# Kernel optimization log

Hardware: AMD Instinct MI355X
Metric: run time of the kernel (lower is better)

Reference implementation:

```python
import jax, jax.numpy as jnp
import numpy as np

N_NODES = 131072
N_EDGES = 2097152
F_IN = 128
G_NODES = 256  # nodes per graph (equal-size graphs -> ptr = arange(0, N+1, 256))


def _linear(x, W, b):
    return x @ W + b


def _gin_conv(x, src, dst, W1, b1, W2, b2):
    # GINConv with eps=0: MLP(x + sum_{j->i} x_j)
    agg = jax.ops.segment_sum(x[src], dst, num_segments=x.shape[0])
    h = jax.nn.relu(_linear(x + agg, W1, b1))
    return _linear(h, W2, b2)


def _init(key, fan_in, fan_out):
    kw, kb = jax.random.split(key)
    s = 1.0 / np.sqrt(fan_in)
    W = jax.random.uniform(kw, (fan_in, fan_out), jnp.float32, -s, s)
    b = jax.random.uniform(kb, (fan_out,), jnp.float32, -s, s)
    return W, b


def setup_inputs() -> dict:
    key = jax.random.key(0)
    ks = jax.random.split(key, 14)
    x = jax.random.normal(ks[0], (N_NODES, F_IN), jnp.float32)
    edge_index = jax.random.randint(ks[1], (2, N_EDGES), 0, N_NODES, jnp.int64)
    W1a, b1a = _init(ks[2], F_IN, 128)
    W2a, b2a = _init(ks[3], 128, 128)
    W1b, b1b = _init(ks[4], 128, 128)
    W2b, b2b = _init(ks[5], 128, 128)
    Ws1, bs1 = _init(ks[6], 128, 32)
    Ws2, bs2 = _init(ks[7], 32, 32)
    Ws3, bs3 = _init(ks[8], 32, 32)
    Wm1, bm1 = _init(ks[9], 32 * 32, 32)
    Wm2, bm2 = _init(ks[10], 32, 32)
    Wm3, bm3 = _init(ks[11], 32, 2)
    return dict(x=x, edge_index=edge_index,
                W1a=W1a, b1a=b1a, W2a=W2a, b2a=b2a,
                W1b=W1b, b1b=b1b, W2b=W2b, b2b=b2b,
                Ws1=Ws1, bs1=bs1, Ws2=Ws2, bs2=bs2, Ws3=Ws3, bs3=bs3,
                Wm1=Wm1, bm1=bm1, Wm2=Wm2, bm2=bm2, Wm3=Wm3, bm3=bm3,
                nodes_per_graph=G_NODES)


def reference(x, edge_index, W1a, b1a, W2a, b2a, W1b, b1b, W2b, b2b,
              Ws1, bs1, Ws2, bs2, Ws3, bs3,
              Wm1, bm1, Wm2, bm2, Wm3, bm3, nodes_per_graph):
    src, dst = edge_index[0], edge_index[1]
    # two GINConv layers, each followed by outer ReLU (as in forward)
    h = jax.nn.relu(_gin_conv(x, src, dst, W1a, b1a, W2a, b2a))
    h = jax.nn.relu(_gin_conv(h, src, dst, W1b, b1b, W2b, b2b))
    # dropout is identity in eval mode; F.normalize(dim=1) row-wise L2
    hn = h / jnp.maximum(jnp.linalg.norm(h, axis=1, keepdims=True), 1e-12)
    s = jax.nn.relu(_linear(hn, Ws1, bs1))
    s = jax.nn.relu(_linear(s, Ws2, bs2))
    s = jax.nn.relu(_linear(s, Ws3, bs3))  # [N, 32]
    G = x.shape[0] // nodes_per_graph
    sg = s.reshape(G, nodes_per_graph, 32)
    # per-graph second-order pooling: graph.T @ graph, flattened
    HH = jnp.einsum('gnf,gne->gfe', sg, sg).reshape(G, 32 * 32)  # [G, 1024]
    o = jax.nn.relu(_linear(HH, Wm1, bm1))
    o = jax.nn.relu(_linear(o, Wm2, bm2))
    out = jax.nn.relu(_linear(o, Wm3, bm3))  # [G, 2]; output dropout identity in eval
    return (HH, out)
```

## Files before the change

### kernel.cpp

```cpp
#include <hip/hip_runtime.h>
#include <hip/hip_bf16.h>


#define NN 131072
#define NE 2097152
#define NG 512
#define NB 1024
#define BCAP 4096
#define ECH 8192
#define CAP 3072

typedef unsigned short u16;
typedef unsigned int u32;
typedef __attribute__((ext_vector_type(8))) short short8;
typedef __attribute__((ext_vector_type(4))) float f32x4;

__device__ __forceinline__ float bf2f(u16 u) {
    union { u32 i; float f; } x; x.i = ((u32)u) << 16; return x.f;
}
__device__ __forceinline__ u16 f2bf(float f) {
    union { u32 i; float f; } x; x.f = f;
    u32 r = x.i + 0x7fffu + ((x.i >> 16) & 1u);
    return (u16)(r >> 16);
}

__global__ __launch_bounds__(256) void cast_x(const float* __restrict__ xf,
                                              u16* __restrict__ xb) {
    int i = blockIdx.x * 256 + threadIdx.x;
    const float4* src = (const float4*)xf;
    float4 a = src[2 * i], b = src[2 * i + 1];
    uint4 o;
    o.x = (u32)f2bf(a.x) | ((u32)f2bf(a.y) << 16);
    o.y = (u32)f2bf(a.z) | ((u32)f2bf(a.w) << 16);
    o.z = (u32)f2bf(b.x) | ((u32)f2bf(b.y) << 16);
    o.w = (u32)f2bf(b.z) | ((u32)f2bf(b.w) << 16);
    ((uint4*)xb)[i] = o;
}

__global__ __launch_bounds__(256) void init_cursor(int* __restrict__ cursor) {
    int b = blockIdx.x * 256 + threadIdx.x;
    cursor[b] = b * BCAP;
}

__global__ __launch_bounds__(256) void bin_scatter(const int* __restrict__ gsrc,
                                                   const int* __restrict__ gdst,
                                                   int* __restrict__ cursor,
                                                   u32* __restrict__ ebuf) {
    __shared__ int lc[NB];
    __shared__ int rb[NB];
    __shared__ int lb[NB];
    int t = threadIdx.x;
    for (int i = 0; i < 4; ++i) lc[t + i * 256] = 0;
    __syncthreads();
    int base = blockIdx.x * ECH;
    for (int i = 0; i < ECH / 256; ++i) {
        int d = gdst[base + i * 256 + t];
        atomicAdd(&lc[d >> 7], 1);
    }
    __syncthreads();
    for (int i = 0; i < 4; ++i) {
        int b = t + i * 256;
        int c = lc[b];
        rb[b] = c ? atomicAdd(&cursor[b], c) : 0;
        lb[b] = 0;
    }
    __syncthreads();
    for (int i = 0; i < ECH / 256; ++i) {
        int idx = base + i * 256 + t;
        int d = gdst[idx];
        int s = gsrc[idx];
        int b = d >> 7;
        int o = atomicAdd(&lb[b], 1);
        ebuf[rb[b] + o] = ((u32)s << 7) | (u32)(d & 127);
    }
}

__global__ __launch_bounds__(512) void aggregate_bucket(const u16* __restrict__ X,
                                                        const u32* __restrict__ ebuf,
                                                        const int* __restrict__ bcur,
                                                        u16* __restrict__ T) {
    __shared__ int lcnt[128];
    __shared__ int lstart[128];
    __shared__ int lofs[128];
    __shared__ int sorted[CAP];
    int t = threadIdx.x, lane = t & 63, wave = t >> 6;
    int bkt = blockIdx.x;
    const u32* Xu = (const u32*)X;

    float a0[16], a1[16];
#pragma unroll
    for (int i = 0; i < 16; ++i) {
        int row = bkt * 128 + wave * 16 + i;
        u32 v = Xu[(size_t)row * 64 + lane];
        a0[i] = bf2f((u16)v);
        a1[i] = bf2f((u16)(v >> 16));
    }

    int e0 = bkt * BCAP, e1 = bcur[bkt];
    for (int cs = e0; cs < e1; cs += CAP) {
        int n = min(CAP, e1 - cs);
        if (t < 128) lcnt[t] = 0;
        __syncthreads();
        for (int j = t; j < n; j += 512)
            atomicAdd(&lcnt[ebuf[cs + j] & 127], 1);
        __syncthreads();
        if (wave == 0) {
            int c0 = lcnt[2 * lane], c1 = lcnt[2 * lane + 1];
            int s = c0 + c1, e = s;
            for (int o = 1; o < 64; o <<= 1) {
                int u = __shfl_up(e, o, 64);
                if (lane >= o) e += u;
            }
            int excl = e - s;
            lstart[2 * lane] = excl;          lofs[2 * lane] = excl;
            lstart[2 * lane + 1] = excl + c0; lofs[2 * lane + 1] = excl + c0;
        }
        __syncthreads();
        for (int j = t; j < n; j += 512) {
            u32 e = ebuf[cs + j];
            int pos = atomicAdd(&lofs[e & 127], 1);
            sorted[pos] = (int)(e >> 7);
        }
        __syncthreads();
#pragma unroll
        for (int i = 0; i < 16; ++i) {
            int node = wave * 16 + i;
            int p = lstart[node], pe = p + lcnt[node];
            for (; p < pe; p += 8) {
                int s[8]; float m[8];
#pragma unroll
                for (int k = 0; k < 8; ++k) {
                    int q = p + k;
                    s[k] = sorted[q < pe ? q : pe - 1];
                    m[k] = (q < pe) ? 1.f : 0.f;
                }
                u32 w[8];
#pragma unroll
                for (int k = 0; k < 8; ++k) w[k] = Xu[(size_t)s[k] * 64 + lane];
#pragma unroll
                for (int k = 0; k < 8; ++k) {
                    a0[i] = fmaf(m[k], bf2f((u16)w[k]), a0[i]);
                    a1[i] = fmaf(m[k], bf2f((u16)(w[k] >> 16)), a1[i]);
                }
            }
        }
        __syncthreads();
    }

    u32* Tu = (u32*)T;
#pragma unroll
    for (int i = 0; i < 16; ++i) {
        int row = bkt * 128 + wave * 16 + i;
        Tu[(size_t)row * 64 + lane] = (u32)f2bf(a0[i]) | ((u32)f2bf(a1[i]) << 16);
    }
}

__global__ __launch_bounds__(256) void transpose_w(const float* a, const float* b,
                                                   const float* c, const float* d, u16* Wt) {
    const float* w = (blockIdx.x == 0) ? a : (blockIdx.x == 1) ? b : (blockIdx.x == 2) ? c : d;
    u16* o = Wt + blockIdx.x * 16384;
    for (int i = 0; i < 64; ++i) {
        int idx = threadIdx.x + i * 256;
        o[(idx & 127) * 128 + (idx >> 7)] = f2bf(w[idx]);
    }
}

__global__ __launch_bounds__(256) void transpose_small(const float* Ws1, const float* Ws2,
                                                       const float* Ws3, u16* Wsm) {
    int t = threadIdx.x;
    for (int i = 0; i < 16; ++i) {
        int idx = t + i * 256;
        int k = idx >> 5, n = idx & 31;
        Wsm[n * 128 + k] = f2bf(Ws1[idx]);
    }
    for (int i = 0; i < 4; ++i) {
        int idx = t + i * 256;
        int k = idx >> 5, n = idx & 31;
        Wsm[4096 + n * 32 + k] = f2bf(Ws2[idx]);
        Wsm[5120 + n * 32 + k] = f2bf(Ws3[idx]);
    }
}

__global__ __launch_bounds__(256) void gemm2_relu(const u16* __restrict__ A,
                                                  const u16* __restrict__ Wt1,
                                                  const u16* __restrict__ Wt2,
                                                  const float* __restrict__ b1,
                                                  const float* __restrict__ b2,
                                                  u16* __restrict__ C) {
    __shared__ u16 As[64][136];
    __shared__ u16 Ws[128][136];
    int tid = threadIdx.x;
    size_t rowBase = (size_t)blockIdx.x * 64;

    uint4 w2r[8];
#pragma unroll
    for (int i = 0; i < 8; ++i) {
        int c = tid + i * 256;
        w2r[i] = *(const uint4*)(Wt2 + (c >> 4) * 128 + ((c & 15) << 3));
    }
    for (int i = 0; i < 4; ++i) {
        int c = tid + i * 256;
        int r = c >> 4, co = (c & 15) << 3;
        *(uint4*)&As[r][co] = *(const uint4*)(A + (rowBase + r) * 128 + co);
    }
    for (int i = 0; i < 8; ++i) {
        int c = tid + i * 256;
        int r = c >> 4, co = (c & 15) << 3;
        *(uint4*)&Ws[r][co] = *(const uint4*)(Wt1 + r * 128 + co);
    }
    __syncthreads();

    int lane = tid & 63, wave = tid >> 6;
    int quad = lane >> 4, l16 = lane & 15;

    f32x4 acc[8];
#pragma unroll
    for (int t = 0; t < 8; ++t) acc[t] = (f32x4){0.f, 0.f, 0.f, 0.f};
#pragma unroll
    for (int c = 0; c < 4; ++c) {
        short8 a = *(const short8*)&As[wave * 16 + l16][c * 32 + quad * 8];
#pragma unroll
        for (int t = 0; t < 8; ++t) {
            short8 b = *(const short8*)&Ws[t * 16 + l16][c * 32 + quad * 8];
            acc[t] = __builtin_amdgcn_mfma_f32_16x16x32_bf16(a, b, acc[t], 0, 0, 0);
        }
    }

#pragma unroll
    for (int t = 0; t < 8; ++t) {
        int col = t * 16 + l16;
        float bv = b1[col];
#pragma unroll
        for (int r = 0; r < 4; ++r)
            As[wave * 16 + quad * 4 + r][col] = f2bf(fmaxf(acc[t][r] + bv, 0.f));
    }
    __syncthreads();

#pragma unroll
    for (int i = 0; i < 8; ++i) {
        int c = tid + i * 256;
        *(uint4*)&Ws[c >> 4][(c & 15) << 3] = w2r[i];
    }
    __syncthreads();

    f32x4 acc2[8];
#pragma unroll
    for (int t = 0; t < 8; ++t) acc2[t] = (f32x4){0.f, 0.f, 0.f, 0.f};
#pragma unroll
    for (int c = 0; c < 4; ++c) {
        short8 a = *(const short8*)&As[wave * 16 + l16][c * 32 + quad * 8];
#pragma unroll
        for (int t = 0; t < 8; ++t) {
            short8 b = *(const short8*)&Ws[t * 16 + l16][c * 32 + quad * 8];
            acc2[t] = __builtin_amdgcn_mfma_f32_16x16x32_bf16(a, b, acc2[t], 0, 0, 0);
        }
    }
#pragma unroll
    for (int t = 0; t < 8; ++t) {
        int col = t * 16 + l16;
        float bv = b2[col];
#pragma unroll
        for (int r = 0; r < 4; ++r) {
            int row = wave * 16 + quad * 4 + r;
            C[(rowBase + row) * 128 + col] = f2bf(fmaxf(acc2[t][r] + bv, 0.f));
        }
    }
}

__global__ __launch_bounds__(256) void norm_mlp_mfma(const u16* __restrict__ X,
                                                     const u16* __restrict__ Wsm,
                                                     const float* __restrict__ bs1,
                                                     const float* __restrict__ bs2,
                                                     const float* __restrict__ bs3,
                                                     float* __restrict__ S) {
    __shared__ u16 As[64][136];
    __shared__ u16 W1s[32][136];
    __shared__ u16 W23s[2][32][40];
    __shared__ u16 H[64][40];
    int tid = threadIdx.x, lane = tid & 63, wave = tid >> 6;
    int quad = lane >> 4, l16 = lane & 15;
    size_t rowBase = (size_t)blockIdx.x * 64;

#pragma unroll
    for (int i = 0; i < 2; ++i) {
        int c = tid + i * 256;
        int r = c >> 4, co = (c & 15) << 3;
        *(uint4*)&W1s[r][co] = *(const uint4*)(Wsm + r * 128 + co);
    }
    {
        int which = tid >> 7, cc = tid & 127;
        int r = cc >> 2, co = (cc & 3) << 3;
        *(uint4*)&W23s[which][r][co] = *(const uint4*)(Wsm + 4096 + which * 1024 + r * 32 + co);
    }

    const u32* Xu = (const u32*)X;
    for (int i = 0; i < 16; ++i) {
        int row = wave * 16 + i;
        u32 v = Xu[(rowBase + row) * 64 + lane];
        float f0 = bf2f((u16)v), f1 = bf2f((u16)(v >> 16));
        float ss = f0 * f0 + f1 * f1;
        for (int o = 1; o < 64; o <<= 1) ss += __shfl_xor(ss, o, 64);
        float inv = 1.0f / fmaxf(sqrtf(ss), 1e-12f);
        *(u32*)&As[row][2 * lane] = (u32)f2bf(f0 * inv) | ((u32)f2bf(f1 * inv) << 16);
    }
    __syncthreads();

    f32x4 acc[2];
    acc[0] = (f32x4){0.f, 0.f, 0.f, 0.f};
    acc[1] = (f32x4){0.f, 0.f, 0.f, 0.f};
#pragma unroll
    for (int c = 0; c < 4; ++c) {
        short8 a = *(const short8*)&As[wave * 16 + l16][c * 32 + quad * 8];
#pragma unroll
        for (int t = 0; t < 2; ++t) {
            short8 b = *(const short8*)&W1s[t * 16 + l16][c * 32 + quad * 8];
            acc[t] = __builtin_amdgcn_mfma_f32_16x16x32_bf16(a, b, acc[t], 0, 0, 0);
        }
    }
#pragma unroll
    for (int t = 0; t < 2; ++t) {
        int col = t * 16 + l16;
        float bv = bs1[col];
#pragma unroll
        for (int r = 0; r < 4; ++r)
            H[wave * 16 + quad * 4 + r][col] = f2bf(fmaxf(acc[t][r] + bv, 0.f));
    }
    __syncthreads();

    f32x4 acc2[2];
    acc2[0] = (f32x4){0.f, 0.f, 0.f, 0.f};
    acc2[1] = (f32x4){0.f, 0.f, 0.f, 0.f};
    {
        short8 a = *(const short8*)&H[wave * 16 + l16][quad * 8];
#pragma unroll
        for (int t = 0; t < 2; ++t) {
            short8 b = *(const short8*)&W23s[0][t * 16 + l16][quad * 8];
            acc2[t] = __builtin_amdgcn_mfma_f32_16x16x32_bf16(a, b, acc2[t], 0, 0, 0);
        }
    }
    __syncthreads();
#pragma unroll
    for (int t = 0; t < 2; ++t) {
        int col = t * 16 + l16;
        float bv = bs2[col];
#pragma unroll
        for (int r = 0; r < 4; ++r)
            H[wave * 16 + quad * 4 + r][col] = f2bf(fmaxf(acc2[t][r] + bv, 0.f));
    }
    __syncthreads();

    f32x4 acc3[2];
    acc3[0] = (f32x4){0.f, 0.f, 0.f, 0.f};
    acc3[1] = (f32x4){0.f, 0.f, 0.f, 0.f};
    {
        short8 a = *(const short8*)&H[wave * 16 + l16][quad * 8];
#pragma unroll
        for (int t = 0; t < 2; ++t) {
            short8 b = *(const short8*)&W23s[1][t * 16 + l16][quad * 8];
            acc3[t] = __builtin_amdgcn_mfma_f32_16x16x32_bf16(a, b, acc3[t], 0, 0, 0);
        }
    }
#pragma unroll
    for (int t = 0; t < 2; ++t) {
        int col = t * 16 + l16;
        float bv = bs3[col];
#pragma unroll
        for (int r = 0; r < 4; ++r) {
            int row = wave * 16 + quad * 4 + r;
            S[(rowBase + row) * 32 + col] = fmaxf(acc3[t][r] + bv, 0.f);
        }
    }
}

__global__ __launch_bounds__(256) void gram(const float* __restrict__ S,
                                            float* __restrict__ out) {
    __shared__ float Sg[256 * 32];
    int t = threadIdx.x, g = blockIdx.x;
    const float4* src = (const float4*)(S + (size_t)g * 8192);
    float4* dst = (float4*)Sg;
    for (int i = 0; i < 8; ++i) dst[t + i * 256] = src[t + i * 256];
    __syncthreads();

    int f = t >> 3, e0 = (t & 7) << 2;
    float4 a = {0.f, 0.f, 0.f, 0.f};
    for (int n = 0; n < 256; ++n) {
        float sf = Sg[n * 32 + f];
        float4 se = *(const float4*)&Sg[n * 32 + e0];
        a.x += sf * se.x; a.y += sf * se.y; a.z += sf * se.z; a.w += sf * se.w;
    }
    *(float4*)(out + (size_t)g * 1024 + f * 32 + e0) = a;
}

__global__ __launch_bounds__(256) void graph_mlp(const float* __restrict__ HH,
                                                 const float* Wm1, const float* bm1,
                                                 const float* Wm2, const float* bm2,
                                                 const float* Wm3, const float* bm3,
                                                 float* __restrict__ out) {
    __shared__ float hh[1024];
    __shared__ float red[256];
    __shared__ float o1[32];
    __shared__ float o2[32];
    int t = threadIdx.x, g = blockIdx.x;
    ((float4*)hh)[t] = ((const float4*)(HH + (size_t)g * 1024))[t];
    __syncthreads();

    int j = t & 31, part = t >> 5;
    float p = 0.f;
    for (int i = 0; i < 128; ++i) { int k = part * 128 + i; p += hh[k] * Wm1[k * 32 + j]; }
    red[t] = p;
    __syncthreads();
    if (t < 32) {
        float s = 0.f;
        for (int q = 0; q < 8; ++q) s += red[q * 32 + t];
        o1[t] = fmaxf(s + bm1[t], 0.f);
    }
    __syncthreads();
    if (t < 32) {
        float s = 0.f;
        for (int k = 0; k < 32; ++k) s += o1[k] * Wm2[k * 32 + t];
        o2[t] = fmaxf(s + bm2[t], 0.f);
    }
    __syncthreads();
    if (t < 2) {
        float s = 0.f;
        for (int k = 0; k < 32; ++k) s += o2[k] * Wm3[k * 2 + t];
        out[524288 + g * 2 + t] = fmaxf(s + bm3[t], 0.f);
    }
}

extern "C" void kernel_launch(void* const* d_in, const int* in_sizes, int n_in,
                              void* d_out, int out_size, void* d_ws, size_t ws_size,
                              hipStream_t stream) {
    const float* x   = (const float*)d_in[0];
    const int*   ei  = (const int*)d_in[1];
    const float* W1a = (const float*)d_in[2];  const float* b1a = (const float*)d_in[3];
    const float* W2a = (const float*)d_in[4];  const float* b2a = (const float*)d_in[5];
    const float* W1b = (const float*)d_in[6];  const float* b1b = (const float*)d_in[7];
    const float* W2b = (const float*)d_in[8];  const float* b2b = (const float*)d_in[9];
    const float* Ws1 = (const float*)d_in[10]; const float* bs1 = (const float*)d_in[11];
    const float* Ws2 = (const float*)d_in[12]; const float* bs2 = (const float*)d_in[13];
    const float* Ws3 = (const float*)d_in[14]; const float* bs3 = (const float*)d_in[15];
    const float* Wm1 = (const float*)d_in[16]; const float* bm1 = (const float*)d_in[17];
    const float* Wm2 = (const float*)d_in[18]; const float* bm2 = (const float*)d_in[19];
    const float* Wm3 = (const float*)d_in[20]; const float* bm3 = (const float*)d_in[21];
    float* out = (float*)d_out;

    const int* gsrc = ei;
    const int* gdst = ei + NE;

    char* ws = (char*)d_ws;
    size_t off = 0;
    auto alloc = [&](size_t bytes) { size_t r = off; off = (off + bytes + 255) & ~(size_t)255; return r; };
    int*  cursor = (int*)(ws + alloc((size_t)NB * 4));
    u32*  ebuf   = (u32*)(ws + alloc((size_t)NB * BCAP * 4));
    u16*  Wt     = (u16*)(ws + alloc(4 * 16384 * 2));
    u16*  Wsm    = (u16*)(ws + alloc(6144 * 2));
    u16*  X0     = (u16*)(ws + alloc((size_t)NN * 128 * 2));
    u16*  B1     = (u16*)(ws + alloc((size_t)NN * 128 * 2));
    float* S     = (float*)B1;
    (void)ws_size; (void)n_in; (void)in_sizes; (void)out_size;

    init_cursor<<<NB / 256, 256, 0, stream>>>(cursor);
    bin_scatter<<<NE / ECH, 256, 0, stream>>>(gsrc, gdst, cursor, ebuf);

    cast_x<<<NN * 128 / (256 * 8), 256, 0, stream>>>(x, X0);
    transpose_w<<<4, 256, 0, stream>>>(W1a, W2a, W1b, W2b, Wt);
    transpose_small<<<1, 256, 0, stream>>>(Ws1, Ws2, Ws3, Wsm);

    aggregate_bucket<<<NB, 512, 0, stream>>>(X0, ebuf, cursor, B1);
    gemm2_relu<<<NN / 64, 256, 0, stream>>>(B1, Wt + 0 * 16384, Wt + 1 * 16384, b1a, b2a, X0);
    aggregate_bucket<<<NB, 512, 0, stream>>>(X0, ebuf, cursor, B1);
    gemm2_relu<<<NN / 64, 256, 0, stream>>>(B1, Wt + 2 * 16384, Wt + 3 * 16384, b1b, b2b, X0);

    norm_mlp_mfma<<<NN / 64, 256, 0, stream>>>(X0, Wsm, bs1, bs2, bs3, S);
    gram<<<NG, 256, 0, stream>>>(S, out);
    graph_mlp<<<NG, 256, 0, stream>>>(out, Wm1, bm1, Wm2, bm2, Wm3, bm3, out);
}
```

Measured before the change: 499.4 us.

## Build padded CSR once and fuse aggregation into GIN MLP kernel

Adds a csr_sort kernel that sorts each bucket's edges by destination once into a padded CSR. Padding entries point to a zeroed sentinel row NN, so the gather loop needs no masking. The per-layer bucket sort is dropped, and the neighbour-sum gather is fused into the two-GEMM MLP kernel, which now works on 128-row tiles with 512 threads. This removes the per-layer re-sort, the bf16 intermediate write and reload, and a kernel launch. In exchange it adds capacity limits (ECAP/CCAP) that could overflow on skewed degree distributions, and the fused kernel may lose occupancy.

```diff
diff --git a/kernel.cpp b/kernel.cpp
--- a/kernel.cpp
+++ b/kernel.cpp
@@ -6,9 +6,9 @@
 #define NE 2097152
 #define NG 512
 #define NB 1024
-#define BCAP 4096
+#define ECAP 2560
+#define CCAP 3328
 #define ECH 8192
-#define CAP 3072
 
 typedef unsigned short u16;
 typedef unsigned int u32;
@@ -37,9 +37,17 @@
     ((uint4*)xb)[i] = o;
 }
 
+__global__ __launch_bounds__(128) void zero_tail(u16* __restrict__ X0,
+                                                 u16* __restrict__ H1) {
+    int t = threadIdx.x;
+    u32* a = (u32*)(X0 + (size_t)NN * 128);
+    u32* b = (u32*)(H1 + (size_t)NN * 128);
+    if (t < 64) a[t] = 0; else b[t - 64] = 0;
+}
+
 __global__ __launch_bounds__(256) void init_cursor(int* __restrict__ cursor) {
     int b = blockIdx.x * 256 + threadIdx.x;
-    cursor[b] = b * BCAP;
+    cursor[b] = b * ECAP;
 }
 
 __global__ __launch_bounds__(256) void bin_scatter(const int* __restrict__ gsrc,
@@ -75,83 +83,50 @@
     }
 }
 
-__global__ __launch_bounds__(512) void aggregate_bucket(const u16* __restrict__ X,
-                                                        const u32* __restrict__ ebuf,
-                                                        const int* __restrict__ bcur,
-                                                        u16* __restrict__ T) {
+__global__ __launch_bounds__(512) void csr_sort(const u32* __restrict__ ebuf,
+                                                const int* __restrict__ cursor,
+                                                int* __restrict__ csr,
+                                                int* __restrict__ start,
+                                                int* __restrict__ deg) {
     __shared__ int lcnt[128];
     __shared__ int lstart[128];
     __shared__ int lofs[128];
-    __shared__ int sorted[CAP];
     int t = threadIdx.x, lane = t & 63, wave = t >> 6;
     int bkt = blockIdx.x;
-    const u32* Xu = (const u32*)X;
-
-    float a0[16], a1[16];
-#pragma unroll
-    for (int i = 0; i < 16; ++i) {
-        int row = bkt * 128 + wave * 16 + i;
-        u32 v = Xu[(size_t)row * 64 + lane];
-        a0[i] = bf2f((u16)v);
-        a1[i] = bf2f((u16)(v >> 16));
-    }
-
-    int e0 = bkt * BCAP, e1 = bcur[bkt];
-    for (int cs = e0; cs < e1; cs += CAP) {
-        int n = min(CAP, e1 - cs);
-        if (t < 128) lcnt[t] = 0;
-        __syncthreads();
-        for (int j = t; j < n; j += 512)
-            atomicAdd(&lcnt[ebuf[cs + j] & 127], 1);
-        __syncthreads();
-        if (wave == 0) {
-            int c0 = lcnt[2 * lane], c1 = lcnt[2 * lane + 1];
-            int s = c0 + c1, e = s;
-            for (int o = 1; o < 64; o <<= 1) {
-                int u = __shfl_up(e, o, 64);
-                if (lane >= o) e += u;
-            }
-            int excl = e - s;
-            lstart[2 * lane] = excl;          lofs[2 * lane] = excl;
-            lstart[2 * lane + 1] = excl + c0; lofs[2 * lane + 1] = excl + c0;
-        }
-        __syncthreads();
-        for (int j = t; j < n; j += 512) {
-            u32 e = ebuf[cs + j];
-            int pos = atomicAdd(&lofs[e & 127], 1);
-            sorted[pos] = (int)(e >> 7);
-        }
-        __syncthreads();
-#pragma unroll
-        for (int i = 0; i < 16; ++i) {
-            int node = wave * 16 + i;
-            int p = lstart[node], pe = p + lcnt[node];
-            for (; p < pe; p += 8) {
-                int s[8]; float m[8];
-#pragma unroll
-                for (int k = 0; k < 8; ++k) {
-                    int q = p + k;
-                    s[k] = sorted[q < pe ? q : pe - 1];
-                    m[k] = (q < pe) ? 1.f : 0.f;
-                }
-                u32 w[8];
-#pragma unroll
-                for (int k = 0; k < 8; ++k) w[k] = Xu[(size_t)s[k] * 64 + lane];
-#pragma unroll
-                for (int k = 0; k < 8; ++k) {
-                    a0[i] = fmaf(m[k], bf2f((u16)w[k]), a0[i]);
-                    a1[i] = fmaf(m[k], bf2f((u16)(w[k] >> 16)), a1[i]);
-                }
-            }
-        }
-        __syncthreads();
-    }
-
-    u32* Tu = (u32*)T;
-#pragma unroll
-    for (int i = 0; i < 16; ++i) {
-        int row = bkt * 128 + wave * 16 + i;
-        Tu[(size_t)row * 64 + lane] = (u32)f2bf(a0[i]) | ((u32)f2bf(a1[i]) << 16);
+    int e0 = bkt * ECAP;
+    int n = cursor[bkt] - e0;
+    if (t < 128) lcnt[t] = 0;
+    __syncthreads();
+    for (int j = t; j < n; j += 512)
+        atomicAdd(&lcnt[ebuf[e0 + j] & 127], 1);
+    __syncthreads();
+    if (wave == 0) {
+        int c0 = lcnt[2 * lane], c1 = lcnt[2 * lane + 1];
+        int r0 = (c0 + 7) & ~7, r1 = (c1 + 7) & ~7;
+        int s = r0 + r1, e = s;
+        for (int o = 1; o < 64; o <<= 1) {
+            int u = __shfl_up(e, o, 64);
+            if (lane >= o) e += u;
+        }
+        int excl = e - s;
+        lstart[2 * lane] = excl;          lofs[2 * lane] = excl;
+        lstart[2 * lane + 1] = excl + r0; lofs[2 * lane + 1] = excl + r0;
+    }
+    __syncthreads();
+    for (int j = t; j < n; j += 512) {
+        u32 e = ebuf[e0 + j];
+        int node = e & 127;
+        int pos = atomicAdd(&lofs[node], 1);
+        csr[bkt * CCAP + pos] = (int)(e >> 7);
+    }
+    __syncthreads();
+    if (t < 128) {
+        int c = lcnt[t];
+        int cp = (c + 7) & ~7;
+        int base = bkt * CCAP + lstart[t];
+        for (int q = c; q < cp; ++q) csr[base + q] = NN;
+        start[bkt * 128 + t] = base;
+        deg[bkt * 128 + t] = cp;
     }
 }
 
@@ -181,37 +156,58 @@
     }
 }
 
-__global__ __launch_bounds__(256) void gemm2_relu(const u16* __restrict__ A,
+__global__ __launch_bounds__(512, 4) void agg_mlp(const u16* __restrict__ X,
+                                                  const int* __restrict__ csr,
+                                                  const int* __restrict__ start,
+                                                  const int* __restrict__ deg,
                                                   const u16* __restrict__ Wt1,
                                                   const u16* __restrict__ Wt2,
                                                   const float* __restrict__ b1,
                                                   const float* __restrict__ b2,
                                                   u16* __restrict__ C) {
-    __shared__ u16 As[64][136];
+    __shared__ u16 As[128][136];
     __shared__ u16 Ws[128][136];
-    int tid = threadIdx.x;
-    size_t rowBase = (size_t)blockIdx.x * 64;
-
-    uint4 w2r[8];
-#pragma unroll
-    for (int i = 0; i < 8; ++i) {
-        int c = tid + i * 256;
-        w2r[i] = *(const uint4*)(Wt2 + (c >> 4) * 128 + ((c & 15) << 3));
-    }
+    int tid = threadIdx.x, lane = tid & 63, wave = tid >> 6;
+    int quad = lane >> 4, l16 = lane & 15;
+    size_t rowBase = (size_t)blockIdx.x * 128;
+    const u32* Xu = (const u32*)X;
+
+#pragma unroll
     for (int i = 0; i < 4; ++i) {
-        int c = tid + i * 256;
-        int r = c >> 4, co = (c & 15) << 3;
-        *(uint4*)&As[r][co] = *(const uint4*)(A + (rowBase + r) * 128 + co);
-    }
-    for (int i = 0; i < 8; ++i) {
-        int c = tid + i * 256;
+        int c = tid + i * 512;
         int r = c >> 4, co = (c & 15) << 3;
         *(uint4*)&Ws[r][co] = *(const uint4*)(Wt1 + r * 128 + co);
     }
-    __syncthreads();
-
-    int lane = tid & 63, wave = tid >> 6;
-    int quad = lane >> 4, l16 = lane & 15;
+
+    for (int i = 0; i < 16; ++i) {
+        int row = (int)rowBase + wave * 16 + i;
+        u32 v = Xu[(row << 6) + lane];
+        float a0 = bf2f((u16)v), a1 = bf2f((u16)(v >> 16));
+        int st = start[row], de = deg[row];
+        const int* ip = csr + st;
+        for (int p = 0; p < de; p += 8) {
+            int4 i0 = *(const int4*)(ip + p);
+            int4 i1 = *(const int4*)(ip + p + 4);
+            int s[8] = {i0.x, i0.y, i0.z, i0.w, i1.x, i1.y, i1.z, i1.w};
+            u32 w[8];
+#pragma unroll
+            for (int k = 0; k < 8; ++k) w[k] = Xu[(s[k] << 6) + lane];
+#pragma unroll
+            for (int k = 0; k < 8; ++k) {
+                a0 += bf2f((u16)w[k]);
+                a1 += bf2f((u16)(w[k] >> 16));
+            }
+        }
+        *(u32*)&As[wave * 16 + i][2 * lane] = (u32)f2bf(a0) | ((u32)f2bf(a1) << 16);
+    }
+    __syncthreads();
+
+    uint4 w2r[4];
+#pragma unroll
+    for (int i = 0; i < 4; ++i) {
+        int c = tid + i * 512;
+        w2r[i] = *(const uint4*)(Wt2 + (c >> 4) * 128 + ((c & 15) << 3));
+    }
 
     f32x4 acc[8];
 #pragma unroll
@@ -225,7 +221,6 @@
             acc[t] = __builtin_amdgcn_mfma_f32_16x16x32_bf16(a, b, acc[t], 0, 0, 0);
         }
     }
-
 #pragma unroll
     for (int t = 0; t < 8; ++t) {
         int col = t * 16 + l16;
@@ -237,8 +232,8 @@
     __syncthreads();
 
 #pragma unroll
-    for (int i = 0; i < 8; ++i) {
-        int c = tid + i * 256;
+    for (int i = 0; i < 4; ++i) {
+        int c = tid + i * 512;
         *(uint4*)&Ws[c >> 4][(c & 15) << 3] = w2r[i];
     }
     __syncthreads();
@@ -452,25 +447,30 @@
     size_t off = 0;
     auto alloc = [&](size_t bytes) { size_t r = off; off = (off + bytes + 255) & ~(size_t)255; return r; };
     int*  cursor = (int*)(ws + alloc((size_t)NB * 4));
-    u32*  ebuf   = (u32*)(ws + alloc((size_t)NB * BCAP * 4));
+    u32*  ebuf   = (u32*)(ws + alloc((size_t)NB * ECAP * 4));
+    int*  csr    = (int*)(ws + alloc((size_t)NB * CCAP * 4));
+    int*  stA    = (int*)(ws + alloc((size_t)NN * 4));
+    int*  dgA    = (int*)(ws + alloc((size_t)NN * 4));
     u16*  Wt     = (u16*)(ws + alloc(4 * 16384 * 2));
     u16*  Wsm    = (u16*)(ws + alloc(6144 * 2));
-    u16*  X0     = (u16*)(ws + alloc((size_t)NN * 128 * 2));
-    u16*  B1     = (u16*)(ws + alloc((size_t)NN * 128 * 2));
-    float* S     = (float*)B1;
+    u16*  X0     = (u16*)(ws + alloc((size_t)(NN + 1) * 128 * 2));
+    u16*  H1     = (u16*)(ws + alloc((size_t)(NN + 1) * 128 * 2));
+    float* S     = (float*)ebuf;
     (void)ws_size; (void)n_in; (void)in_sizes; (void)out_size;
 
     init_cursor<<<NB / 256, 256, 0, stream>>>(cursor);
     bin_scatter<<<NE / ECH, 256, 0, stream>>>(gsrc, gdst, cursor, ebuf);
+    csr_sort<<<NB, 512, 0, stream>>>(ebuf, cursor, csr, stA, dgA);
 
     cast_x<<<NN * 128 / (256 * 8), 256, 0, stream>>>(x, X0);
+    zero_tail<<<1, 128, 0, stream>>>(X0, H1);
     transpose_w<<<4, 256, 0, stream>>>(W1a, W2a, W1b, W2b, Wt);
     transpose_small<<<1, 256, 0, stream>>>(Ws1, Ws2, Ws3, Wsm);
 
-    aggregate_bucket<<<NB, 512, 0, stream>>>(X0, ebuf, cursor, B1);
-    gemm2_relu<<<NN / 64, 256, 0, stream>>>(B1, Wt + 0 * 16384, Wt + 1 * 16384, b1a, b2a, X0);
-    aggregate_bucket<<<NB, 512, 0, stream>>>(X0, ebuf, cursor, B1);
-    gemm2_relu<<<NN / 64, 256, 0, stream>>>(B1, Wt + 2 * 16384, Wt + 3 * 16384, b1b, b2b, X0);
+    agg_mlp<<<NN / 128, 512, 0, stream>>>(X0, csr, stA, dgA,
+                                          Wt + 0 * 16384, Wt + 1 * 16384, b1a, b2a, H1);
+    agg_mlp<<<NN / 128, 512, 0, stream>>>(H1, csr, stA, dgA,
+                                          Wt + 2 * 16384, Wt + 3 * 16384, b1b, b2b, X0);
 
     norm_mlp_mfma<<<NN / 64, 256, 0, stream>>>(X0, Wsm, bs1, bs2, bs3, S);
     gram<<<NG, 256, 0, stream>>>(S, out);
```

Result: no change. 505.0 us (+1.1%).
